# Performance work log

Hardware: AMD Instinct MI355X
Metric: run time of the kernel (lower is better)

## Reference

```python
import jax, jax.numpy as jnp
import numpy as np

B, P, CV = 2, 1024, 768
V, DNB, K = 50000, 300, 3
H = 768  # max(512, v_dim)
TOTAL_IN = CV + K * DNB + K  # include_scores=True
EPS = 1e-12


def setup_inputs() -> dict:
    key = jax.random.key(0)
    ks = jax.random.split(key, 7)
    v_seq = jax.random.normal(ks[0], (B, P, CV), dtype=jnp.float32)
    T = jax.random.normal(ks[1], (V, CV), dtype=jnp.float32)
    T_clip = T / jnp.linalg.norm(T, axis=-1, keepdims=True)  # bank rows are L2-normalized
    nb_vecs = jax.random.normal(ks[2], (V, DNB), dtype=jnp.float32)
    W1 = jax.random.normal(ks[3], (TOTAL_IN, H), dtype=jnp.float32) * (1.0 / np.sqrt(TOTAL_IN))
    b1 = jnp.zeros((H,), dtype=jnp.float32)
    W2 = jax.random.normal(ks[4], (H, CV), dtype=jnp.float32) * (1.0 / np.sqrt(H))
    b2 = jnp.zeros((CV,), dtype=jnp.float32)
    return {"v_seq": v_seq, "T_clip": T_clip, "nb_vecs": nb_vecs,
            "W1": W1, "b1": b1, "W2": W2, "b2": b2}


def _layer_norm(x, eps=1e-5):
    mu = jnp.mean(x, axis=-1, keepdims=True)
    var = jnp.var(x, axis=-1, keepdims=True)
    return (x - mu) * jax.lax.rsqrt(var + eps)


def reference(v_seq, T_clip, nb_vecs, W1, b1, W2, b2):
    # --- retrieve (no_grad in original) ---
    q = v_seq / jnp.maximum(jnp.linalg.norm(v_seq, axis=-1, keepdims=True), EPS)
    S = jnp.einsum('bpc,vc->bpv', q, T_clip)            # (B,P,V) cosine sims
    val, idx = jax.lax.top_k(S, K)                       # (B,P,K) each
    nb_sel = nb_vecs[idx]                                # gather -> (B,P,K,DNB)
    # --- fuse_concat ---
    nb_flat = nb_sel.reshape(B, P, K * DNB)
    combined = jnp.concatenate([v_seq, nb_flat, val], axis=-1)  # (B,P,TOTAL_IN)
    h = jax.nn.gelu(combined @ W1 + b1, approximate=False)      # nn.GELU default = erf
    fused = h @ W2 + b2                                          # dropout inactive (eval)
    return _layer_norm(fused)                                    # F.layer_norm, no affine
```

## Files before the change

kernel.cpp:

```cpp
#include <hip/hip_runtime.h>
#include <hip/hip_bf16.h>

typedef unsigned short u16;
typedef unsigned int u32;
typedef __attribute__((ext_vector_type(4))) unsigned short u16x4;
typedef __attribute__((ext_vector_type(8))) unsigned short u16x8;
typedef __attribute__((ext_vector_type(8))) short bf16x8;
typedef __attribute__((ext_vector_type(4))) float f32x4;

#define ROWS 2048
#define CV 768
#define VOCAB 50000
#define NPAD 50176
#define NTILES 196
#define NSEG 392
#define NSEGP 392
#define DNB 300
#define TOTAL_IN 1671
#define KPAD1 1696
#define HD 768
#define NT 12

__device__ __forceinline__ u16 f2bf(float f) {
  union { __hip_bfloat16 h; u16 u; } x;
  x.h = __float2bfloat16(f);
  return x.u;
}

__device__ __forceinline__ u16 bfkey(u16 u) {
  return (u & 0x8000) ? (u16)~u : (u16)(u | 0x8000);
}

__device__ __forceinline__ void gload16(const u16* g, const u16* l) {
  __builtin_amdgcn_global_load_lds(
      (const __attribute__((address_space(1))) void*)g,
      (__attribute__((address_space(3))) void*)l, 16, 0, 0);
}

__device__ __forceinline__ float block_sum256(float v, float* ws) {
#pragma unroll
  for (int off = 32; off > 0; off >>= 1) v += __shfl_xor(v, off, 64);
  int tid = threadIdx.x;
  if ((tid & 63) == 0) ws[tid >> 6] = v;
  __syncthreads();
  float s = ws[0] + ws[1] + ws[2] + ws[3];
  __syncthreads();
  return s;
}

__global__ __launch_bounds__(256) void normalize_kernel(
    const float* __restrict__ v_seq, float* __restrict__ q, u16* __restrict__ q16) {
  __shared__ float ws[4];
  int row = blockIdx.x, tid = threadIdx.x;
  const float* x = v_seq + (size_t)row * CV;
  float x0 = x[tid], x1 = x[tid + 256], x2 = x[tid + 512];
  float s = block_sum256(x0 * x0 + x1 * x1 + x2 * x2, ws);
  float denom = fmaxf(sqrtf(s), 1e-12f);
  float q0 = x0 / denom, q1 = x1 / denom, q2 = x2 / denom;
  float* qr = q + (size_t)row * CV;
  u16* qb = q16 + (size_t)row * CV;
  qr[tid] = q0; qr[tid + 256] = q1; qr[tid + 512] = q2;
  qb[tid] = f2bf(q0); qb[tid + 256] = f2bf(q1); qb[tid + 512] = f2bf(q2);
}

__global__ __launch_bounds__(256) void cvt_bf16_kernel(
    const float* __restrict__ src, u16* __restrict__ dst, int n4) {
  int i = blockIdx.x * 256 + threadIdx.x;
  int stride = gridDim.x * 256;
  for (; i < n4; i += stride) {
    float4 v = reinterpret_cast<const float4*>(src)[i];
    u16x4 o = {f2bf(v.x), f2bf(v.y), f2bf(v.z), f2bf(v.w)};
    reinterpret_cast<u16x4*>(dst)[i] = o;
  }
}

__global__ __launch_bounds__(256) void transpose_cvt_kernel(
    const float* __restrict__ src, u16* __restrict__ dst, int Ksrc, int ldk, int N) {
  __shared__ float tile[32][33];
  int tx = threadIdx.x & 31, ty = threadIdx.x >> 5;
  int kb = blockIdx.x * 32, nb = blockIdx.y * 32;
#pragma unroll
  for (int i = 0; i < 4; ++i) {
    int k = kb + ty + i * 8, n = nb + tx;
    tile[ty + i * 8][tx] = (k < Ksrc) ? src[(size_t)k * N + n] : 0.f;
  }
  __syncthreads();
#pragma unroll
  for (int i = 0; i < 4; ++i) {
    int n = nb + ty + i * 8, k = kb + tx;
    dst[(size_t)n * ldk + k] = f2bf(tile[tx][ty + i * 8]);
  }
}

__global__ __launch_bounds__(512, 2) void score_gemm_256(
    const u16* __restrict__ q16, const u16* __restrict__ T16,
    u16* __restrict__ S16, u16* __restrict__ segmax) {
  __shared__ __align__(16) u16 lds[65536];
  __shared__ float smx[256][4];

  int tid = threadIdx.x;
  int w = tid >> 6, lane = tid & 63;
  int wr = w >> 2, wc = w & 3;
  int l15 = lane & 15, l4 = lane >> 4;

  int bid = blockIdx.x;
  int wg = (bid & 7) * NTILES + (bid >> 3);
  int mtile = wg & 7, ntile = wg >> 3;
  int m0 = mtile * 256, n0 = ntile * 256;

  int t8 = tid >> 3;
  int jcol = (((tid & 7) ^ (t8 & 7)) << 3);
  int rowA = m0 + t8;
  int rowB0 = n0 + t8;        rowB0 = rowB0 > (VOCAB - 1) ? (VOCAB - 1) : rowB0;
  int rowB1 = n0 + 64 + t8;   rowB1 = rowB1 > (VOCAB - 1) ? (VOCAB - 1) : rowB1;
  int rowB2 = n0 + 128 + t8;  rowB2 = rowB2 > (VOCAB - 1) ? (VOCAB - 1) : rowB2;
  int rowB3 = n0 + 192 + t8;  rowB3 = rowB3 > (VOCAB - 1) ? (VOCAB - 1) : rowB3;
  int w512 = w * 512;

  int xorv = (l15 & 7) << 4;
  int l416 = l4 << 4;
  int c0 = ((l416) ^ xorv) >> 1;
  int c1 = ((64 + l416) ^ xorv) >> 1;
  int aro = (wr * 128 + l15) * 64;
  int bro = 16384 + (wc * 64 + l15) * 64;

  f32x4 acc[8][4];
#pragma unroll
  for (int i = 0; i < 8; ++i)
#pragma unroll
    for (int j = 0; j < 4; ++j) acc[i][j] = {0.f, 0.f, 0.f, 0.f};

  bf16x8 af[2][4], bfr[2][4];

#define STAGE_A(R0) gload16(q16 + (size_t)(rowA + (R0)) * CV + ktn + jcol, \
                            &lds[nbase + (R0) * 64 + w512])
#define STAGE_B0() gload16(T16 + (size_t)rowB0 * CV + ktn + jcol, &lds[nbase + 16384 + w512])
#define STAGE_B1() gload16(T16 + (size_t)rowB1 * CV + ktn + jcol, &lds[nbase + 16384 + 4096 + w512])
#define STAGE_B2() gload16(T16 + (size_t)rowB2 * CV + ktn + jcol, &lds[nbase + 16384 + 8192 + w512])
#define STAGE_B3() gload16(T16 + (size_t)rowB3 * CV + ktn + jcol, &lds[nbase + 16384 + 12288 + w512])

#define LDA4(MIB)                                                           \
  _Pragma("unroll") for (int ks = 0; ks < 2; ++ks)                          \
  _Pragma("unroll") for (int mi = 0; mi < 4; ++mi)                          \
    af[ks][mi] = *reinterpret_cast<const bf16x8*>(                          \
        &lds[cbase + aro + ((MIB) + mi) * 1024 + (ks ? c1 : c0)]);

#define LDB2(NIB)                                                           \
  _Pragma("unroll") for (int ks = 0; ks < 2; ++ks)                          \
  _Pragma("unroll") for (int ni = 0; ni < 2; ++ni)                          \
    bfr[ks][(NIB) + ni] = *reinterpret_cast<const bf16x8*>(                 \
        &lds[cbase + bro + ((NIB) + ni) * 1024 + (ks ? c1 : c0)]);

#define MFMAQ(MIB, NIB)                                                     \
  _Pragma("unroll") for (int mi = 0; mi < 4; ++mi)                          \
  _Pragma("unroll") for (int ni = 0; ni < 2; ++ni) {                        \
    acc[(MIB) + mi][(NIB) + ni] = __builtin_amdgcn_mfma_f32_16x16x32_bf16(  \
        af[0][mi], bfr[0][(NIB) + ni], acc[(MIB) + mi][(NIB) + ni], 0, 0, 0); \
    acc[(MIB) + mi][(NIB) + ni] = __builtin_amdgcn_mfma_f32_16x16x32_bf16(  \
        af[1][mi], bfr[1][(NIB) + ni], acc[(MIB) + mi][(NIB) + ni], 0, 0, 0); \
  }

  {
    int nbase = 0, ktn = 0;
    STAGE_B0(); STAGE_B1(); STAGE_B2(); STAGE_B3();
    STAGE_A(0); STAGE_A(128); STAGE_A(64); STAGE_A(192);
  }

  for (int t = 0; t < NT; ++t) {
    int cb = t & 1;
    int cbase = cb * 32768;
    int nbase = cbase ^ 32768;
    int ktn = ((t + 1 < NT) ? (t + 1) : t) * 64;

    asm volatile("s_waitcnt vmcnt(2)" ::: "memory");
    __builtin_amdgcn_s_barrier();

    LDA4(0)
    LDB2(0)
    STAGE_B0(); STAGE_B1();
    __builtin_amdgcn_s_barrier();
    __builtin_amdgcn_s_setprio(1);
    MFMAQ(0, 0)
    __builtin_amdgcn_s_setprio(0);
    __builtin_amdgcn_s_barrier();

    LDB2(2)
    STAGE_B2(); STAGE_B3();
    __builtin_amdgcn_s_barrier();
    __builtin_amdgcn_s_setprio(1);
    MFMAQ(0, 2)
    __builtin_amdgcn_s_setprio(0);
    asm volatile("s_waitcnt vmcnt(4)" ::: "memory");
    __builtin_amdgcn_s_barrier();

    LDA4(4)
    STAGE_A(0); STAGE_A(128);
    __builtin_amdgcn_s_barrier();
    __builtin_amdgcn_s_setprio(1);
    MFMAQ(4, 0)
    __builtin_amdgcn_s_setprio(0);
    __builtin_amdgcn_s_barrier();

    STAGE_A(64); STAGE_A(192);
    __builtin_amdgcn_s_setprio(1);
    MFMAQ(4, 2)
    __builtin_amdgcn_s_setprio(0);
  }
  asm volatile("s_waitcnt vmcnt(0)" ::: "memory");
  __builtin_amdgcn_s_barrier();

#pragma unroll
  for (int mi = 0; mi < 8; ++mi)
#pragma unroll
    for (int ni = 0; ni < 4; ++ni) {
      int gr = m0 + wr * 128 + mi * 16 + l4 * 4;
      int gc = n0 + wc * 64 + ni * 16 + l15;
#pragma unroll
      for (int r = 0; r < 4; ++r)
        S16[(size_t)(gr + r) * NPAD + gc] = f2bf(acc[mi][ni][r]);
    }

#pragma unroll
  for (int mi = 0; mi < 8; ++mi)
#pragma unroll
    for (int r = 0; r < 4; ++r) {
      float v = -3e38f;
#pragma unroll
      for (int ni = 0; ni < 4; ++ni) {
        bool ok = (n0 + wc * 64 + ni * 16 + l15) < VOCAB;
        v = fmaxf(v, ok ? acc[mi][ni][r] : -3e38f);
      }
#pragma unroll
      for (int d = 1; d < 16; d <<= 1) v = fmaxf(v, __shfl_xor(v, d, 64));
      if (l15 == 0) smx[wr * 128 + mi * 16 + l4 * 4 + r][wc] = v;
    }
  __syncthreads();
  if (tid < 256) {
    float s0 = fmaxf(smx[tid][0], smx[tid][1]);
    float s1 = fmaxf(smx[tid][2], smx[tid][3]);
    segmax[(size_t)(m0 + tid) * NSEGP + 2 * ntile]     = bfkey(f2bf(s0));
    segmax[(size_t)(m0 + tid) * NSEGP + 2 * ntile + 1] = bfkey(f2bf(s1));
  }
#undef STAGE_A
#undef STAGE_B0
#undef STAGE_B1
#undef STAGE_B2
#undef STAGE_B3
#undef LDA4
#undef LDB2
#undef MFMAQ
}

template <int ACT, int OUTBF>
__global__ __launch_bounds__(256) void gemm_bt(
    const u16* __restrict__ A, int lda,
    const u16* __restrict__ B, int ldb, int nclamp,
    int Kdim, const float* __restrict__ bias,
    float* __restrict__ Cf, u16* __restrict__ Cb, int ldc) {
  __shared__ __align__(16) u16 Asm[128 * 32];
  __shared__ __align__(16) u16 Bsm[128 * 32];
  int tid = threadIdx.x;
  int w = tid >> 6, lane = tid & 63;
  int wr = w >> 1, wc = w & 1;
  int m0 = blockIdx.x * 128;
  int n0 = blockIdx.y * 128;
  f32x4 acc[4][4];
#pragma unroll
  for (int i = 0; i < 4; ++i)
#pragma unroll
    for (int j = 0; j < 4; ++j) acc[i][j] = {0.f, 0.f, 0.f, 0.f};

  int r0 = tid >> 2, s0 = tid & 3;
  int b0r = n0 + r0;       b0r = b0r > nclamp ? nclamp : b0r;
  int b1r = n0 + 64 + r0;  b1r = b1r > nclamp ? nclamp : b1r;

  for (int k0 = 0; k0 < Kdim; k0 += 32) {
    __syncthreads();
    gload16(A + (size_t)(m0 + r0) * lda + k0 + s0 * 8, Asm + w * 512);
    gload16(A + (size_t)(m0 + 64 + r0) * lda + k0 + s0 * 8, Asm + 2048 + w * 512);
    gload16(B + (size_t)b0r * ldb + k0 + s0 * 8, Bsm + w * 512);
    gload16(B + (size_t)b1r * ldb + k0 + s0 * 8, Bsm + 2048 + w * 512);
    __syncthreads();
    int l15 = lane & 15, l4 = lane >> 4;
    bf16x8 af[4], bfr[4];
#pragma unroll
    for (int mi = 0; mi < 4; ++mi)
      af[mi] = *reinterpret_cast<const bf16x8*>(Asm + (wr * 64 + mi * 16 + l15) * 32 + l4 * 8);
#pragma unroll
    for (int ni = 0; ni < 4; ++ni)
      bfr[ni] = *reinterpret_cast<const bf16x8*>(Bsm + (wc * 64 + ni * 16 + l15) * 32 + l4 * 8);
#pragma unroll
    for (int mi = 0; mi < 4; ++mi)
#pragma unroll
      for (int ni = 0; ni < 4; ++ni)
        acc[mi][ni] = __builtin_amdgcn_mfma_f32_16x16x32_bf16(af[mi], bfr[ni], acc[mi][ni], 0, 0, 0);
  }

  int l15 = lane & 15, l4 = lane >> 4;
#pragma unroll
  for (int mi = 0; mi < 4; ++mi) {
#pragma unroll
    for (int ni = 0; ni < 4; ++ni) {
      int gr = m0 + wr * 64 + mi * 16 + l4 * 4;
      int gc = n0 + wc * 64 + ni * 16 + l15;
      float bv = bias ? bias[gc] : 0.f;
#pragma unroll
      for (int r = 0; r < 4; ++r) {
        float x = acc[mi][ni][r] + bv;
        if (ACT) x = 0.5f * x * (1.0f + erff(x * 0.70710678118654752f));
        size_t co = (size_t)(gr + r) * ldc + gc;
        if (OUTBF) Cb[co] = f2bf(x);
        else       Cf[co] = x;
      }
    }
  }
}

__global__ __launch_bounds__(256) void segsel_topk(
    const u16* __restrict__ segmax, const u16* __restrict__ S,
    int* __restrict__ cidx) {
  __shared__ u32 skey[448];
  __shared__ u32 winners[16];
  __shared__ u32 cl[256][16];
  int row = blockIdx.x, tid = threadIdx.x;

  if (tid < 224) {
#pragma unroll
    for (int j = 0; j < 2; ++j) {
      int s = tid * 2 + j;
      u32 k = 0;
      if (s < NSEG) k = ((u32)segmax[(size_t)row * NSEGP + s] << 9) | (u32)(511 - s);
      skey[s] = k;
    }
  }
  __syncthreads();

  if (tid < 64) {
    u32 v[7];
#pragma unroll
    for (int j = 0; j < 7; ++j) v[j] = skey[tid + 64 * j];
#pragma unroll
    for (int rd = 0; rd < 16; ++rd) {
      u32 m = v[0];
#pragma unroll
      for (int j = 1; j < 7; ++j) m = (v[j] > m) ? v[j] : m;
#pragma unroll
      for (int d = 1; d < 64; d <<= 1) {
        u32 o = (u32)__shfl_xor((int)m, d, 64);
        m = (o > m) ? o : m;
      }
#pragma unroll
      for (int j = 0; j < 7; ++j) v[j] = (v[j] == m) ? 0u : v[j];
      if (tid == 0) winners[rd] = m;
    }
  }
  __syncthreads();

  int wi = tid >> 4, off = (tid & 15) * 8;
  int seg = 511 - (int)(winners[wi] & 511);
  const u16* Sr = S + (size_t)row * NPAD + seg * 128 + off;
  u16x8 vv = *reinterpret_cast<const u16x8*>(Sr);
  u32 ck[8];
  int gbase = seg * 128 + off;
#pragma unroll
  for (int jj = 0; jj < 8; ++jj) {
    int g = gbase + jj;
    u32 c = ((u32)bfkey(vv[jj]) << 16) | (u32)(0xFFFF - g);
    ck[jj] = (g >= VOCAB) ? 0u : c;
  }
#define CE(i, j) { u32 a = ck[i], b = ck[j]; ck[i] = a > b ? a : b; ck[j] = a > b ? b : a; }
  CE(0,1) CE(2,3) CE(4,5) CE(6,7)
  CE(0,2) CE(1,3) CE(4,6) CE(5,7)
  CE(1,2) CE(5,6)
  CE(0,4) CE(1,5) CE(2,6) CE(3,7)
  CE(2,4) CE(3,5)
  CE(1,2) CE(3,4) CE(5,6)
#undef CE
#pragma unroll
  for (int k = 0; k < 8; ++k) cl[tid][k] = ck[k];
#pragma unroll
  for (int k = 8; k < 16; ++k) cl[tid][k] = 0u;
  __syncthreads();

  for (int s = 128; s >= 1; s >>= 1) {
    if (tid < s) {
      u32 ov[16];
      int pa = 0, pb = 0;
#pragma unroll
      for (int k = 0; k < 16; ++k) {
        u32 va = cl[tid][pa], vb = cl[tid + s][pb];
        bool ta = va >= vb;
        ov[k] = ta ? va : vb;
        pa += ta ? 1 : 0;
        pb += ta ? 0 : 1;
      }
#pragma unroll
      for (int k = 0; k < 16; ++k) cl[tid][k] = ov[k];
    }
    __syncthreads();
  }
  if (tid < 16) cidx[(size_t)row * 16 + tid] = 0xFFFF - (int)(cl[0][tid] & 0xFFFF);
}

__global__ __launch_bounds__(256) void rescore_kernel(
    const float* __restrict__ q, const float* __restrict__ T,
    const int* __restrict__ cidx,
    float* __restrict__ val, int* __restrict__ idx) {
  __shared__ float sex[16];
  int row = blockIdx.x, tid = threadIdx.x;
  int wv = tid >> 6, lane = tid & 63;
  const float* __restrict__ qr = q + (size_t)row * CV;
#pragma unroll
  for (int c0 = 0; c0 < 4; ++c0) {
    int c = wv + c0 * 4;
    int n = cidx[(size_t)row * 16 + c];
    const float* tr = T + (size_t)n * CV;
    float part = 0.f;
    int kb = lane * 12;
#pragma unroll
    for (int j3 = 0; j3 < 3; ++j3) {
      float4 a = *reinterpret_cast<const float4*>(tr + kb + j3 * 4);
      float4 b = *reinterpret_cast<const float4*>(qr + kb + j3 * 4);
      part += a.x * b.x + a.y * b.y + a.z * b.z + a.w * b.w;
    }
#pragma unroll
    for (int off = 32; off >= 1; off >>= 1) part += __shfl_xor(part, off, 64);
    if (lane == 0) sex[c] = part;
  }
  __syncthreads();
  if (tid == 0) {
    float xv[16]; int xi[16];
#pragma unroll
    for (int c = 0; c < 16; ++c) { xv[c] = sex[c]; xi[c] = cidx[(size_t)row * 16 + c]; }
    for (int t = 0; t < 3; ++t) {
      float bv = -__builtin_inff(); int bi = 0x7fffffff, bc = -1;
#pragma unroll
      for (int c = 0; c < 16; ++c) {
        if (xi[c] < 0) continue;
        if (xv[c] > bv || (xv[c] == bv && xi[c] < bi)) { bv = xv[c]; bi = xi[c]; bc = c; }
      }
      val[row * 3 + t] = bv;
      idx[row * 3 + t] = bi;
      xi[bc] = -1;
    }
  }
}

__global__ __launch_bounds__(256) void gather_concat_kernel(
    const float* __restrict__ v_seq, const float* __restrict__ nb,
    const float* __restrict__ val, const int* __restrict__ idx,
    u16* __restrict__ c16) {
  int row = blockIdx.x, tid = threadIdx.x;
  u16* c = c16 + (size_t)row * KPAD1;
  const float* vs = v_seq + (size_t)row * CV;
  if (tid < 192) {
    float4 v = *reinterpret_cast<const float4*>(vs + tid * 4);
    u16x4 o = {f2bf(v.x), f2bf(v.y), f2bf(v.z), f2bf(v.w)};
    *reinterpret_cast<u16x4*>(c + tid * 4) = o;
  }
  int i0 = idx[row * 3 + 0], i1 = idx[row * 3 + 1], i2 = idx[row * 3 + 2];
  if (tid < 75) {
    float4 v = *reinterpret_cast<const float4*>(nb + (size_t)i0 * DNB + tid * 4);
    u16x4 o = {f2bf(v.x), f2bf(v.y), f2bf(v.z), f2bf(v.w)};
    *reinterpret_cast<u16x4*>(c + CV + tid * 4) = o;
    v = *reinterpret_cast<const float4*>(nb + (size_t)i1 * DNB + tid * 4);
    o = {f2bf(v.x), f2bf(v.y), f2bf(v.z), f2bf(v.w)};
    *reinterpret_cast<u16x4*>(c + CV + DNB + tid * 4) = o;
    v = *reinterpret_cast<const float4*>(nb + (size_t)i2 * DNB + tid * 4);
    o = {f2bf(v.x), f2bf(v.y), f2bf(v.z), f2bf(v.w)};
    *reinterpret_cast<u16x4*>(c + CV + 2 * DNB + tid * 4) = o;
  }
  if (tid < 28) {
    int o = CV + 3 * DNB + tid;
    c[o] = (tid < 3) ? f2bf(val[row * 3 + tid]) : (u16)0;
  }
}

__global__ __launch_bounds__(256) void layernorm_kernel(float* __restrict__ C) {
  __shared__ float ws[4];
  int row = blockIdx.x, tid = threadIdx.x;
  float* x = C + (size_t)row * CV;
  float x0 = x[tid], x1 = x[tid + 256], x2 = x[tid + 512];
  float mu = block_sum256(x0 + x1 + x2, ws) * (1.0f / 768.0f);
  float d0 = x0 - mu, d1 = x1 - mu, d2 = x2 - mu;
  float var = block_sum256(d0 * d0 + d1 * d1 + d2 * d2, ws) * (1.0f / 768.0f);
  float inv = 1.0f / sqrtf(var + 1e-5f);
  x[tid] = d0 * inv; x[tid + 256] = d1 * inv; x[tid + 512] = d2 * inv;
}

extern "C" void kernel_launch(void* const* d_in, const int* in_sizes, int n_in,
                              void* d_out, int out_size, void* d_ws, size_t ws_size,
                              hipStream_t stream) {
  const float* v_seq = (const float*)d_in[0];
  const float* T = (const float*)d_in[1];
  const float* nb = (const float*)d_in[2];
  const float* W1 = (const float*)d_in[3];
  const float* b1 = (const float*)d_in[4];
  const float* W2 = (const float*)d_in[5];
  const float* b2 = (const float*)d_in[6];
  float* out = (float*)d_out;

  char* base = (char*)d_ws;
  size_t off = 0;
  auto alloc = [&](size_t bytes) -> void* {
    void* p = base + off;
    off += (bytes + 255) & ~(size_t)255;
    return p;
  };
  float* q   = (float*)alloc((size_t)ROWS * CV * 4);
  u16* q16   = (u16*)alloc((size_t)ROWS * CV * 2);
  u16* T16   = (u16*)alloc((size_t)VOCAB * CV * 2);
  u16* c16   = (u16*)alloc((size_t)ROWS * KPAD1 * 2);
  u16* h16   = (u16*)alloc((size_t)ROWS * HD * 2);
  u16* W1T   = (u16*)alloc((size_t)HD * KPAD1 * 2);
  u16* W2T   = (u16*)alloc((size_t)HD * HD * 2);
  u16* segmaxb = (u16*)alloc((size_t)ROWS * NSEGP * 2);
  int* cidx   = (int*)alloc((size_t)ROWS * 16 * 4);
  float* val  = (float*)alloc((size_t)ROWS * 3 * 4);
  int* idxb   = (int*)alloc((size_t)ROWS * 3 * 4);
  u16* S16    = (u16*)alloc((size_t)ROWS * NPAD * 2);

  normalize_kernel<<<ROWS, 256, 0, stream>>>(v_seq, q, q16);
  cvt_bf16_kernel<<<2048, 256, 0, stream>>>(T, T16, VOCAB * CV / 4);
  transpose_cvt_kernel<<<dim3(KPAD1 / 32, HD / 32), 256, 0, stream>>>(W1, W1T, TOTAL_IN, KPAD1, HD);
  transpose_cvt_kernel<<<dim3(HD / 32, HD / 32), 256, 0, stream>>>(W2, W2T, HD, HD, HD);

  score_gemm_256<<<8 * NTILES, 512, 0, stream>>>(q16, T16, S16, segmaxb);
  segsel_topk<<<ROWS, 256, 0, stream>>>(segmaxb, S16, cidx);
  rescore_kernel<<<ROWS, 256, 0, stream>>>(q, T, cidx, val, idxb);
  gather_concat_kernel<<<ROWS, 256, 0, stream>>>(v_seq, nb, val, idxb, c16);
  gemm_bt<1, 1><<<dim3(ROWS / 128, HD / 128), 256, 0, stream>>>(
      c16, KPAD1, W1T, KPAD1, HD - 1, KPAD1, b1, nullptr, h16, HD);
  gemm_bt<0, 0><<<dim3(ROWS / 128, HD / 128), 256, 0, stream>>>(
      h16, HD, W2T, HD, HD - 1, HD, b2, out, nullptr, HD);
  layernorm_kernel<<<ROWS, 256, 0, stream>>>(out);
}
```

Measured before the change: 443.8 us.

## Software-pipeline score GEMM with inline-asm LDS reads and fuse rescore with concat

Rewrites the main loop of the score GEMM so it processes two K-tiles per iteration. LDS fragments are read with inline ds_read_b128 at precomputed addresses, and explicit lgkmcnt/vmcnt waits plus sched_barriers interleave the next fragment reads and global staging with the MFMA clusters. The aim is to hide LDS and global load latency behind matrix math. Separately, the rescore and gather/concat kernels are merged so top-3 values and indices stay in shared memory, removing one launch and a global round trip. The hand-tuned wait counts and barriers are fragile: a wrong count would cause races, and forcing the schedule can raise register pressure.

```diff
diff --git a/kernel.cpp b/kernel.cpp
--- a/kernel.cpp
+++ b/kernel.cpp
@@ -117,12 +117,15 @@
   int rowB3 = n0 + 192 + t8;  rowB3 = rowB3 > (VOCAB - 1) ? (VOCAB - 1) : rowB3;
   int w512 = w * 512;
 
-  int xorv = (l15 & 7) << 4;
-  int l416 = l4 << 4;
-  int c0 = ((l416) ^ xorv) >> 1;
-  int c1 = ((64 + l416) ^ xorv) >> 1;
-  int aro = (wr * 128 + l15) * 64;
-  int bro = 16384 + (wc * 64 + l15) * 64;
+  unsigned ldsb = (unsigned)(uintptr_t)(__attribute__((address_space(3))) void*)lds;
+  int x0 = ((l4 ^ (l15 & 7)) << 4);
+  int x1 = (((4 + l4) ^ (l15 & 7)) << 4);
+  int aR = (wr * 128 + l15) * 128;
+  int bR = 32768 + (wc * 64 + l15) * 128;
+  int A0k0 = ldsb + aR + x0, A0k1 = ldsb + aR + x1;
+  int B0k0 = ldsb + bR + x0, B0k1 = ldsb + bR + x1;
+  int A1k0 = A0k0 + 65536, A1k1 = A0k1 + 65536;
+  int B1k0 = B0k0 + 65536, B1k1 = B0k1 + 65536;
 
   f32x4 acc[8][4];
 #pragma unroll
@@ -130,84 +133,97 @@
 #pragma unroll
     for (int j = 0; j < 4; ++j) acc[i][j] = {0.f, 0.f, 0.f, 0.f};
 
-  bf16x8 af[2][4], bfr[2][4];
-
-#define STAGE_A(R0) gload16(q16 + (size_t)(rowA + (R0)) * CV + ktn + jcol, \
-                            &lds[nbase + (R0) * 64 + w512])
-#define STAGE_B0() gload16(T16 + (size_t)rowB0 * CV + ktn + jcol, &lds[nbase + 16384 + w512])
-#define STAGE_B1() gload16(T16 + (size_t)rowB1 * CV + ktn + jcol, &lds[nbase + 16384 + 4096 + w512])
-#define STAGE_B2() gload16(T16 + (size_t)rowB2 * CV + ktn + jcol, &lds[nbase + 16384 + 8192 + w512])
-#define STAGE_B3() gload16(T16 + (size_t)rowB3 * CV + ktn + jcol, &lds[nbase + 16384 + 12288 + w512])
-
-#define LDA4(MIB)                                                           \
-  _Pragma("unroll") for (int ks = 0; ks < 2; ++ks)                          \
-  _Pragma("unroll") for (int mi = 0; mi < 4; ++mi)                          \
-    af[ks][mi] = *reinterpret_cast<const bf16x8*>(                          \
-        &lds[cbase + aro + ((MIB) + mi) * 1024 + (ks ? c1 : c0)]);
-
-#define LDB2(NIB)                                                           \
-  _Pragma("unroll") for (int ks = 0; ks < 2; ++ks)                          \
-  _Pragma("unroll") for (int ni = 0; ni < 2; ++ni)                          \
-    bfr[ks][(NIB) + ni] = *reinterpret_cast<const bf16x8*>(                 \
-        &lds[cbase + bro + ((NIB) + ni) * 1024 + (ks ? c1 : c0)]);
-
-#define MFMAQ(MIB, NIB)                                                     \
-  _Pragma("unroll") for (int mi = 0; mi < 4; ++mi)                          \
-  _Pragma("unroll") for (int ni = 0; ni < 2; ++ni) {                        \
-    acc[(MIB) + mi][(NIB) + ni] = __builtin_amdgcn_mfma_f32_16x16x32_bf16(  \
-        af[0][mi], bfr[0][(NIB) + ni], acc[(MIB) + mi][(NIB) + ni], 0, 0, 0); \
-    acc[(MIB) + mi][(NIB) + ni] = __builtin_amdgcn_mfma_f32_16x16x32_bf16(  \
-        af[1][mi], bfr[1][(NIB) + ni], acc[(MIB) + mi][(NIB) + ni], 0, 0, 0); \
-  }
-
-  {
-    int nbase = 0, ktn = 0;
-    STAGE_B0(); STAGE_B1(); STAGE_B2(); STAGE_B3();
-    STAGE_A(0); STAGE_A(128); STAGE_A(64); STAGE_A(192);
-  }
-
-  for (int t = 0; t < NT; ++t) {
-    int cb = t & 1;
-    int cbase = cb * 32768;
-    int nbase = cbase ^ 32768;
-    int ktn = ((t + 1 < NT) ? (t + 1) : t) * 64;
-
-    asm volatile("s_waitcnt vmcnt(2)" ::: "memory");
-    __builtin_amdgcn_s_barrier();
-
-    LDA4(0)
-    LDB2(0)
-    STAGE_B0(); STAGE_B1();
-    __builtin_amdgcn_s_barrier();
-    __builtin_amdgcn_s_setprio(1);
-    MFMAQ(0, 0)
-    __builtin_amdgcn_s_setprio(0);
-    __builtin_amdgcn_s_barrier();
-
-    LDB2(2)
-    STAGE_B2(); STAGE_B3();
-    __builtin_amdgcn_s_barrier();
-    __builtin_amdgcn_s_setprio(1);
-    MFMAQ(0, 2)
-    __builtin_amdgcn_s_setprio(0);
-    asm volatile("s_waitcnt vmcnt(4)" ::: "memory");
-    __builtin_amdgcn_s_barrier();
-
-    LDA4(4)
-    STAGE_A(0); STAGE_A(128);
-    __builtin_amdgcn_s_barrier();
-    __builtin_amdgcn_s_setprio(1);
-    MFMAQ(4, 0)
-    __builtin_amdgcn_s_setprio(0);
-    __builtin_amdgcn_s_barrier();
-
-    STAGE_A(64); STAGE_A(192);
-    __builtin_amdgcn_s_setprio(1);
-    MFMAQ(4, 2)
-    __builtin_amdgcn_s_setprio(0);
-  }
-  asm volatile("s_waitcnt vmcnt(0)" ::: "memory");
-  __builtin_amdgcn_s_barrier();
+  bf16x8 alo[2][4], ahi[2][4], b01[2][2], b23[2][2];
+
+#define STG(ptr, off16) gload16((ptr), lds + (off16))
+#define STAGE6(NB, KT)                                                        \
+  STG(q16 + (size_t)(rowA) * CV + (KT) + jcol, (NB) + w512);                  \
+  STG(q16 + (size_t)(rowA + 128) * CV + (KT) + jcol, (NB) + 8192 + w512);     \
+  STG(T16 + (size_t)rowB0 * CV + (KT) + jcol, (NB) + 16384 + w512);           \
+  STG(T16 + (size_t)rowB1 * CV + (KT) + jcol, (NB) + 16384 + 4096 + w512);    \
+  STG(T16 + (size_t)rowB2 * CV + (KT) + jcol, (NB) + 16384 + 8192 + w512);    \
+  STG(T16 + (size_t)rowB3 * CV + (KT) + jcol, (NB) + 16384 + 12288 + w512);
+#define STAGE2(NB, KT)                                                        \
+  STG(q16 + (size_t)(rowA + 64) * CV + (KT) + jcol, (NB) + 4096 + w512);      \
+  STG(q16 + (size_t)(rowA + 192) * CV + (KT) + jcol, (NB) + 12288 + w512);
+
+#define DSR(D, B, O) asm volatile("ds_read_b128 %0, %1 offset:" O : "=v"(D) : "v"(B))
+#define READ_B01(K0, K1)                                                      \
+  DSR(b01[0][0], K0, "0"); DSR(b01[0][1], K0, "2048");                        \
+  DSR(b01[1][0], K1, "0"); DSR(b01[1][1], K1, "2048");
+#define READ_B23(K0, K1)                                                      \
+  DSR(b23[0][0], K0, "4096"); DSR(b23[0][1], K0, "6144");                     \
+  DSR(b23[1][0], K1, "4096"); DSR(b23[1][1], K1, "6144");
+#define READ_ALO(K0, K1)                                                      \
+  DSR(alo[0][0], K0, "0"); DSR(alo[0][1], K0, "2048");                        \
+  DSR(alo[0][2], K0, "4096"); DSR(alo[0][3], K0, "6144");                     \
+  DSR(alo[1][0], K1, "0"); DSR(alo[1][1], K1, "2048");                        \
+  DSR(alo[1][2], K1, "4096"); DSR(alo[1][3], K1, "6144");
+#define READ_AHI(K0, K1)                                                      \
+  DSR(ahi[0][0], K0, "8192"); DSR(ahi[0][1], K0, "10240");                    \
+  DSR(ahi[0][2], K0, "12288"); DSR(ahi[0][3], K0, "14336");                   \
+  DSR(ahi[1][0], K1, "8192"); DSR(ahi[1][1], K1, "10240");                    \
+  DSR(ahi[1][2], K1, "12288"); DSR(ahi[1][3], K1, "14336");
+
+#define LGKM(N)                                                               \
+  asm volatile("s_waitcnt lgkmcnt(" N ")" ::: "memory");                      \
+  __builtin_amdgcn_sched_barrier(0)
+#define VMC(N) asm volatile("s_waitcnt vmcnt(" N ")" ::: "memory")
+#define BARX                                                                  \
+  __builtin_amdgcn_sched_barrier(0);                                          \
+  __builtin_amdgcn_s_barrier()
+
+#define CLUSTER(AA, MIB, BB, NIB)                                             \
+  __builtin_amdgcn_s_setprio(1);                                              \
+  _Pragma("unroll") for (int mi = 0; mi < 4; ++mi)                            \
+  _Pragma("unroll") for (int ni = 0; ni < 2; ++ni) {                          \
+    acc[(MIB)+mi][(NIB)+ni] = __builtin_amdgcn_mfma_f32_16x16x32_bf16(        \
+        AA[0][mi], BB[0][ni], acc[(MIB)+mi][(NIB)+ni], 0, 0, 0);              \
+    acc[(MIB)+mi][(NIB)+ni] = __builtin_amdgcn_mfma_f32_16x16x32_bf16(        \
+        AA[1][mi], BB[1][ni], acc[(MIB)+mi][(NIB)+ni], 0, 0, 0);              \
+  }                                                                           \
+  __builtin_amdgcn_s_setprio(0);
+
+  STAGE6(0, 0)
+  STAGE2(0, 0)
+  VMC("2");
+  BARX;
+  READ_ALO(A0k0, A0k1)
+  READ_B01(B0k0, B0k1)
+
+  for (int p = 0; p < 6; ++p) {
+    int kt1 = (2 * p + 1) * 64;
+    int kt2 = (p < 5) ? (2 * p + 2) * 64 : 11 * 64;
+    READ_B23(B0k0, B0k1)
+    STAGE6(32768, kt1)
+    LGKM("4"); CLUSTER(alo, 0, b01, 0) VMC("6"); BARX;
+
+    READ_AHI(A0k0, A0k1)
+    STAGE2(32768, kt1)
+    LGKM("8"); CLUSTER(alo, 0, b23, 2) BARX;
+
+    LGKM("0"); CLUSTER(ahi, 4, b23, 2) VMC("2"); BARX;
+
+    READ_ALO(A1k0, A1k1)
+    READ_B23(B1k0, B1k1)
+    CLUSTER(ahi, 4, b01, 0) BARX;
+    READ_B01(B1k0, B1k1)
+    STAGE6(0, kt2)
+    LGKM("4"); CLUSTER(alo, 0, b23, 2) VMC("6"); BARX;
+
+    READ_AHI(A1k0, A1k1)
+    STAGE2(0, kt2)
+    LGKM("8"); CLUSTER(alo, 0, b01, 0) BARX;
+
+    LGKM("0"); CLUSTER(ahi, 4, b01, 0) VMC("2"); BARX;
+
+    READ_ALO(A0k0, A0k1)
+    READ_B01(B0k0, B0k1)
+    CLUSTER(ahi, 4, b23, 2) BARX;
+  }
+  VMC("0");
+  asm volatile("s_waitcnt lgkmcnt(0)" ::: "memory");
+  __syncthreads();
 
 #pragma unroll
   for (int mi = 0; mi < 8; ++mi)
@@ -241,14 +257,18 @@
     segmax[(size_t)(m0 + tid) * NSEGP + 2 * ntile]     = bfkey(f2bf(s0));
     segmax[(size_t)(m0 + tid) * NSEGP + 2 * ntile + 1] = bfkey(f2bf(s1));
   }
-#undef STAGE_A
-#undef STAGE_B0
-#undef STAGE_B1
-#undef STAGE_B2
-#undef STAGE_B3
-#undef LDA4
-#undef LDB2
-#undef MFMAQ
+#undef STG
+#undef STAGE6
+#undef STAGE2
+#undef DSR
+#undef READ_B01
+#undef READ_B23
+#undef READ_ALO
+#undef READ_AHI
+#undef LGKM
+#undef VMC
+#undef BARX
+#undef CLUSTER
 }
 
 template <int ACT, int OUTBF>
@@ -402,11 +422,13 @@
   if (tid < 16) cidx[(size_t)row * 16 + tid] = 0xFFFF - (int)(cl[0][tid] & 0xFFFF);
 }
 
-__global__ __launch_bounds__(256) void rescore_kernel(
+__global__ __launch_bounds__(256) void rescore_concat(
     const float* __restrict__ q, const float* __restrict__ T,
-    const int* __restrict__ cidx,
-    float* __restrict__ val, int* __restrict__ idx) {
+    const int* __restrict__ cidx, const float* __restrict__ v_seq,
+    const float* __restrict__ nb, u16* __restrict__ c16) {
   __shared__ float sex[16];
+  __shared__ float sval[3];
+  __shared__ int sidx[3];
   int row = blockIdx.x, tid = threadIdx.x;
   int wv = tid >> 6, lane = tid & 63;
   const float* __restrict__ qr = q + (size_t)row * CV;
@@ -439,18 +461,12 @@
         if (xi[c] < 0) continue;
         if (xv[c] > bv || (xv[c] == bv && xi[c] < bi)) { bv = xv[c]; bi = xi[c]; bc = c; }
       }
-      val[row * 3 + t] = bv;
-      idx[row * 3 + t] = bi;
+      sval[t] = bv; sidx[t] = bi;
       xi[bc] = -1;
     }
   }
-}
-
-__global__ __launch_bounds__(256) void gather_concat_kernel(
-    const float* __restrict__ v_seq, const float* __restrict__ nb,
-    const float* __restrict__ val, const int* __restrict__ idx,
-    u16* __restrict__ c16) {
-  int row = blockIdx.x, tid = threadIdx.x;
+  __syncthreads();
+
   u16* c = c16 + (size_t)row * KPAD1;
   const float* vs = v_seq + (size_t)row * CV;
   if (tid < 192) {
@@ -458,7 +474,7 @@
     u16x4 o = {f2bf(v.x), f2bf(v.y), f2bf(v.z), f2bf(v.w)};
     *reinterpret_cast<u16x4*>(c + tid * 4) = o;
   }
-  int i0 = idx[row * 3 + 0], i1 = idx[row * 3 + 1], i2 = idx[row * 3 + 2];
+  int i0 = sidx[0], i1 = sidx[1], i2 = sidx[2];
   if (tid < 75) {
     float4 v = *reinterpret_cast<const float4*>(nb + (size_t)i0 * DNB + tid * 4);
     u16x4 o = {f2bf(v.x), f2bf(v.y), f2bf(v.z), f2bf(v.w)};
@@ -472,7 +488,7 @@
   }
   if (tid < 28) {
     int o = CV + 3 * DNB + tid;
-    c[o] = (tid < 3) ? f2bf(val[row * 3 + tid]) : (u16)0;
+    c[o] = (tid < 3) ? f2bf(sval[tid]) : (u16)0;
   }
 }
 
@@ -516,8 +532,6 @@
   u16* W2T   = (u16*)alloc((size_t)HD * HD * 2);
   u16* segmaxb = (u16*)alloc((size_t)ROWS * NSEGP * 2);
   int* cidx   = (int*)alloc((size_t)ROWS * 16 * 4);
-  float* val  = (float*)alloc((size_t)ROWS * 3 * 4);
-  int* idxb   = (int*)alloc((size_t)ROWS * 3 * 4);
   u16* S16    = (u16*)alloc((size_t)ROWS * NPAD * 2);
 
   normalize_kernel<<<ROWS, 256, 0, stream>>>(v_seq, q, q16);
@@ -527,8 +541,7 @@
 
   score_gemm_256<<<8 * NTILES, 512, 0, stream>>>(q16, T16, S16, segmaxb);
   segsel_topk<<<ROWS, 256, 0, stream>>>(segmaxb, S16, cidx);
-  rescore_kernel<<<ROWS, 256, 0, stream>>>(q, T, cidx, val, idxb);
-  gather_concat_kernel<<<ROWS, 256, 0, stream>>>(v_seq, nb, val, idxb, c16);
+  rescore_concat<<<ROWS, 256, 0, stream>>>(q, T, cidx, v_seq, nb, c16);
   gemm_bt<1, 1><<<dim3(ROWS / 128, HD / 128), 256, 0, stream>>>(
       c16, KPAD1, W1T, KPAD1, HD - 1, KPAD1, b1, nullptr, h16, HD);
   gemm_bt<0, 0><<<dim3(ROWS / 128, HD / 128), 256, 0, stream>>>(
```

After: 622.5 us. +40.3%, slower.

## Compute per-tile top-8 candidates in score GEMM epilogue instead of writing full score matrix

Applied to the files above, without the earlier changes.

The score GEMM no longer writes the full bf16 similarity matrix (about 200 MB) plus segment maxima. Each 256-column tile is staged in LDS, where every thread keeps a per-row top-8 by insertion and pairs of threads merge their lists; only 8 packed key/index candidates per row per tile go to memory. A new merge_topk kernel reduces these candidates to 16 per row. Rescoring and gather/concat are fused into one kernel that uses a stored reciprocal norm instead of a normalized fp32 copy of q. This adds serial insertion-sort work to the GEMM epilogue, but removes the large score-matrix write and reread.

```diff
diff --git a/kernel.cpp b/kernel.cpp
--- a/kernel.cpp
+++ b/kernel.cpp
@@ -13,8 +13,7 @@
 #define VOCAB 50000
 #define NPAD 50176
 #define NTILES 196
-#define NSEG 392
-#define NSEGP 392
+#define CANDW (NTILES * 8)
 #define DNB 300
 #define TOTAL_IN 1671
 #define KPAD1 1696
@@ -49,18 +48,17 @@
 }
 
 __global__ __launch_bounds__(256) void normalize_kernel(
-    const float* __restrict__ v_seq, float* __restrict__ q, u16* __restrict__ q16) {
+    const float* __restrict__ v_seq, float* __restrict__ rinv, u16* __restrict__ q16) {
   __shared__ float ws[4];
   int row = blockIdx.x, tid = threadIdx.x;
   const float* x = v_seq + (size_t)row * CV;
   float x0 = x[tid], x1 = x[tid + 256], x2 = x[tid + 512];
   float s = block_sum256(x0 * x0 + x1 * x1 + x2 * x2, ws);
   float denom = fmaxf(sqrtf(s), 1e-12f);
-  float q0 = x0 / denom, q1 = x1 / denom, q2 = x2 / denom;
-  float* qr = q + (size_t)row * CV;
+  float inv = 1.0f / denom;
   u16* qb = q16 + (size_t)row * CV;
-  qr[tid] = q0; qr[tid + 256] = q1; qr[tid + 512] = q2;
-  qb[tid] = f2bf(q0); qb[tid + 256] = f2bf(q1); qb[tid + 512] = f2bf(q2);
+  qb[tid] = f2bf(x0 * inv); qb[tid + 256] = f2bf(x1 * inv); qb[tid + 512] = f2bf(x2 * inv);
+  if (tid == 0) rinv[row] = inv;
 }
 
 __global__ __launch_bounds__(256) void cvt_bf16_kernel(
@@ -94,9 +92,8 @@
 
 __global__ __launch_bounds__(512, 2) void score_gemm_256(
     const u16* __restrict__ q16, const u16* __restrict__ T16,
-    u16* __restrict__ S16, u16* __restrict__ segmax) {
+    u32* __restrict__ cand) {
   __shared__ __align__(16) u16 lds[65536];
-  __shared__ float smx[256][4];
 
   int tid = threadIdx.x;
   int w = tid >> 6, lane = tid & 63;
@@ -207,39 +204,65 @@
     __builtin_amdgcn_s_setprio(0);
   }
   asm volatile("s_waitcnt vmcnt(0)" ::: "memory");
-  __builtin_amdgcn_s_barrier();
-
-#pragma unroll
-  for (int mi = 0; mi < 8; ++mi)
-#pragma unroll
-    for (int ni = 0; ni < 4; ++ni) {
-      int gr = m0 + wr * 128 + mi * 16 + l4 * 4;
-      int gc = n0 + wc * 64 + ni * 16 + l15;
-#pragma unroll
-      for (int r = 0; r < 4; ++r)
-        S16[(size_t)(gr + r) * NPAD + gc] = f2bf(acc[mi][ni][r]);
-    }
-
-#pragma unroll
-  for (int mi = 0; mi < 8; ++mi)
-#pragma unroll
-    for (int r = 0; r < 4; ++r) {
-      float v = -3e38f;
+  asm volatile("s_waitcnt lgkmcnt(0)" ::: "memory");
+  __syncthreads();
+
+  {
+#pragma unroll
+    for (int mi = 0; mi < 8; ++mi)
 #pragma unroll
       for (int ni = 0; ni < 4; ++ni) {
-        bool ok = (n0 + wc * 64 + ni * 16 + l15) < VOCAB;
-        v = fmaxf(v, ok ? acc[mi][ni][r] : -3e38f);
-      }
-#pragma unroll
-      for (int d = 1; d < 16; d <<= 1) v = fmaxf(v, __shfl_xor(v, d, 64));
-      if (l15 == 0) smx[wr * 128 + mi * 16 + l4 * 4 + r][wc] = v;
-    }
-  __syncthreads();
-  if (tid < 256) {
-    float s0 = fmaxf(smx[tid][0], smx[tid][1]);
-    float s1 = fmaxf(smx[tid][2], smx[tid][3]);
-    segmax[(size_t)(m0 + tid) * NSEGP + 2 * ntile]     = bfkey(f2bf(s0));
-    segmax[(size_t)(m0 + tid) * NSEGP + 2 * ntile + 1] = bfkey(f2bf(s1));
+        int lrb = wr * 128 + mi * 16 + l4 * 4;
+        int lc = wc * 64 + ni * 16 + l15;
+        int gc = n0 + lc;
+        u16* dst = lds + ((lc >> 3) * 256) * 8 + (lc & 7);
+#pragma unroll
+        for (int r = 0; r < 4; ++r) {
+          u16 k = (gc < VOCAB) ? bfkey(f2bf(acc[mi][ni][r])) : (u16)0;
+          dst[(lrb + r) * 8] = k;
+        }
+      }
+    __syncthreads();
+
+    int prow = tid >> 1, half = tid & 1;
+    u32 b[8] = {0, 0, 0, 0, 0, 0, 0, 0};
+    int gcb = ntile * 256 + half * 128;
+#pragma unroll 4
+    for (int i = 0; i < 16; ++i) {
+      u16x8 v = *reinterpret_cast<const u16x8*>(lds + ((half * 16 + i) * 256 + prow) * 8);
+#pragma unroll
+      for (int j = 0; j < 8; ++j) {
+        u32 pk = ((u32)v[j] << 16) | (0xFFFFu ^ (u32)(gcb + i * 8 + j));
+        if (pk > b[7]) {
+          b[7] = pk;
+#pragma unroll
+          for (int k = 7; k > 0; --k) {
+            if (b[k] > b[k - 1]) { u32 tt = b[k]; b[k] = b[k - 1]; b[k - 1] = tt; }
+          }
+        }
+      }
+    }
+    __syncthreads();
+    u32* ex = (u32*)lds;
+#pragma unroll
+    for (int j = 0; j < 8; ++j) ex[tid * 8 + j] = b[j];
+    __syncthreads();
+    if (!half) {
+      const u32* pb = ex + (tid + 1) * 8;
+      u32 o[8];
+      int pa = 0, pq = 0;
+#pragma unroll
+      for (int k = 0; k < 8; ++k) {
+        u32 va = b[pa], vb = pb[pq];
+        bool ta = va >= vb;
+        o[k] = ta ? va : vb;
+        pa += ta ? 1 : 0;
+        pq += ta ? 0 : 1;
+      }
+      u32* cr = cand + (size_t)(m0 + prow) * CANDW + ntile * 8;
+#pragma unroll
+      for (int k = 0; k < 8; ++k) cr[k] = o[k];
+    }
   }
 #undef STAGE_A
 #undef STAGE_B0
@@ -249,6 +272,48 @@
 #undef LDA4
 #undef LDB2
 #undef MFMAQ
+}
+
+__global__ __launch_bounds__(256) void merge_topk(
+    const u32* __restrict__ cand, int* __restrict__ cidx) {
+  __shared__ u32 cl[256][16];
+  int row = blockIdx.x, tid = threadIdx.x;
+  const u32* cr = cand + (size_t)row * CANDW;
+  u32 b[8] = {0, 0, 0, 0, 0, 0, 0, 0};
+  for (int i = tid; i < CANDW; i += 256) {
+    u32 pk = cr[i];
+    if (pk > b[7]) {
+      b[7] = pk;
+#pragma unroll
+      for (int k = 7; k > 0; --k) {
+        if (b[k] > b[k - 1]) { u32 tt = b[k]; b[k] = b[k - 1]; b[k - 1] = tt; }
+      }
+    }
+  }
+#pragma unroll
+  for (int k = 0; k < 8; ++k) cl[tid][k] = b[k];
+#pragma unroll
+  for (int k = 8; k < 16; ++k) cl[tid][k] = 0u;
+  __syncthreads();
+
+  for (int s = 128; s >= 1; s >>= 1) {
+    if (tid < s) {
+      u32 ov[16];
+      int pa = 0, pb = 0;
+#pragma unroll
+      for (int k = 0; k < 16; ++k) {
+        u32 va = cl[tid][pa], vb = cl[tid + s][pb];
+        bool ta = va >= vb;
+        ov[k] = ta ? va : vb;
+        pa += ta ? 1 : 0;
+        pb += ta ? 0 : 1;
+      }
+#pragma unroll
+      for (int k = 0; k < 16; ++k) cl[tid][k] = ov[k];
+    }
+    __syncthreads();
+  }
+  if (tid < 16) cidx[(size_t)row * 16 + tid] = (int)(0xFFFFu ^ (cl[0][tid] & 0xFFFFu));
 }
 
 template <int ACT, int OUTBF>
@@ -316,100 +381,17 @@
   }
 }
 
-__global__ __launch_bounds__(256) void segsel_topk(
-    const u16* __restrict__ segmax, const u16* __restrict__ S,
-    int* __restrict__ cidx) {
-  __shared__ u32 skey[448];
-  __shared__ u32 winners[16];
-  __shared__ u32 cl[256][16];
-  int row = blockIdx.x, tid = threadIdx.x;
-
-  if (tid < 224) {
-#pragma unroll
-    for (int j = 0; j < 2; ++j) {
-      int s = tid * 2 + j;
-      u32 k = 0;
-      if (s < NSEG) k = ((u32)segmax[(size_t)row * NSEGP + s] << 9) | (u32)(511 - s);
-      skey[s] = k;
-    }
-  }
-  __syncthreads();
-
-  if (tid < 64) {
-    u32 v[7];
-#pragma unroll
-    for (int j = 0; j < 7; ++j) v[j] = skey[tid + 64 * j];
-#pragma unroll
-    for (int rd = 0; rd < 16; ++rd) {
-      u32 m = v[0];
-#pragma unroll
-      for (int j = 1; j < 7; ++j) m = (v[j] > m) ? v[j] : m;
-#pragma unroll
-      for (int d = 1; d < 64; d <<= 1) {
-        u32 o = (u32)__shfl_xor((int)m, d, 64);
-        m = (o > m) ? o : m;
-      }
-#pragma unroll
-      for (int j = 0; j < 7; ++j) v[j] = (v[j] == m) ? 0u : v[j];
-      if (tid == 0) winners[rd] = m;
-    }
-  }
-  __syncthreads();
-
-  int wi = tid >> 4, off = (tid & 15) * 8;
-  int seg = 511 - (int)(winners[wi] & 511);
-  const u16* Sr = S + (size_t)row * NPAD + seg * 128 + off;
-  u16x8 vv = *reinterpret_cast<const u16x8*>(Sr);
-  u32 ck[8];
-  int gbase = seg * 128 + off;
-#pragma unroll
-  for (int jj = 0; jj < 8; ++jj) {
-    int g = gbase + jj;
-    u32 c = ((u32)bfkey(vv[jj]) << 16) | (u32)(0xFFFF - g);
-    ck[jj] = (g >= VOCAB) ? 0u : c;
-  }
-#define CE(i, j) { u32 a = ck[i], b = ck[j]; ck[i] = a > b ? a : b; ck[j] = a > b ? b : a; }
-  CE(0,1) CE(2,3) CE(4,5) CE(6,7)
-  CE(0,2) CE(1,3) CE(4,6) CE(5,7)
-  CE(1,2) CE(5,6)
-  CE(0,4) CE(1,5) CE(2,6) CE(3,7)
-  CE(2,4) CE(3,5)
-  CE(1,2) CE(3,4) CE(5,6)
-#undef CE
-#pragma unroll
-  for (int k = 0; k < 8; ++k) cl[tid][k] = ck[k];
-#pragma unroll
-  for (int k = 8; k < 16; ++k) cl[tid][k] = 0u;
-  __syncthreads();
-
-  for (int s = 128; s >= 1; s >>= 1) {
-    if (tid < s) {
-      u32 ov[16];
-      int pa = 0, pb = 0;
-#pragma unroll
-      for (int k = 0; k < 16; ++k) {
-        u32 va = cl[tid][pa], vb = cl[tid + s][pb];
-        bool ta = va >= vb;
-        ov[k] = ta ? va : vb;
-        pa += ta ? 1 : 0;
-        pb += ta ? 0 : 1;
-      }
-#pragma unroll
-      for (int k = 0; k < 16; ++k) cl[tid][k] = ov[k];
-    }
-    __syncthreads();
-  }
-  if (tid < 16) cidx[(size_t)row * 16 + tid] = 0xFFFF - (int)(cl[0][tid] & 0xFFFF);
-}
-
-__global__ __launch_bounds__(256) void rescore_kernel(
-    const float* __restrict__ q, const float* __restrict__ T,
-    const int* __restrict__ cidx,
-    float* __restrict__ val, int* __restrict__ idx) {
+__global__ __launch_bounds__(256) void rescore_concat(
+    const float* __restrict__ v_seq, const float* __restrict__ rinv,
+    const float* __restrict__ T, const int* __restrict__ cidx,
+    const float* __restrict__ nb, u16* __restrict__ c16) {
   __shared__ float sex[16];
+  __shared__ float sval[3];
+  __shared__ int sidx[3];
   int row = blockIdx.x, tid = threadIdx.x;
   int wv = tid >> 6, lane = tid & 63;
-  const float* __restrict__ qr = q + (size_t)row * CV;
+  const float* __restrict__ qr = v_seq + (size_t)row * CV;
+  float ri = rinv[row];
 #pragma unroll
   for (int c0 = 0; c0 < 4; ++c0) {
     int c = wv + c0 * 4;
@@ -425,7 +407,7 @@
     }
 #pragma unroll
     for (int off = 32; off >= 1; off >>= 1) part += __shfl_xor(part, off, 64);
-    if (lane == 0) sex[c] = part;
+    if (lane == 0) sex[c] = part * ri;
   }
   __syncthreads();
   if (tid == 0) {
@@ -439,26 +421,19 @@
         if (xi[c] < 0) continue;
         if (xv[c] > bv || (xv[c] == bv && xi[c] < bi)) { bv = xv[c]; bi = xi[c]; bc = c; }
       }
-      val[row * 3 + t] = bv;
-      idx[row * 3 + t] = bi;
+      sval[t] = bv; sidx[t] = bi;
       xi[bc] = -1;
     }
   }
-}
-
-__global__ __launch_bounds__(256) void gather_concat_kernel(
-    const float* __restrict__ v_seq, const float* __restrict__ nb,
-    const float* __restrict__ val, const int* __restrict__ idx,
-    u16* __restrict__ c16) {
-  int row = blockIdx.x, tid = threadIdx.x;
+  __syncthreads();
+
   u16* c = c16 + (size_t)row * KPAD1;
-  const float* vs = v_seq + (size_t)row * CV;
   if (tid < 192) {
-    float4 v = *reinterpret_cast<const float4*>(vs + tid * 4);
+    float4 v = *reinterpret_cast<const float4*>(qr + tid * 4);
     u16x4 o = {f2bf(v.x), f2bf(v.y), f2bf(v.z), f2bf(v.w)};
     *reinterpret_cast<u16x4*>(c + tid * 4) = o;
   }
-  int i0 = idx[row * 3 + 0], i1 = idx[row * 3 + 1], i2 = idx[row * 3 + 2];
+  int i0 = sidx[0], i1 = sidx[1], i2 = sidx[2];
   if (tid < 75) {
     float4 v = *reinterpret_cast<const float4*>(nb + (size_t)i0 * DNB + tid * 4);
     u16x4 o = {f2bf(v.x), f2bf(v.y), f2bf(v.z), f2bf(v.w)};
@@ -472,7 +447,7 @@
   }
   if (tid < 28) {
     int o = CV + 3 * DNB + tid;
-    c[o] = (tid < 3) ? f2bf(val[row * 3 + tid]) : (u16)0;
+    c[o] = (tid < 3) ? f2bf(sval[tid]) : (u16)0;
   }
 }
 
@@ -507,28 +482,24 @@
     off += (bytes + 255) & ~(size_t)255;
     return p;
   };
-  float* q   = (float*)alloc((size_t)ROWS * CV * 4);
+  float* rinv = (float*)alloc((size_t)ROWS * 4);
   u16* q16   = (u16*)alloc((size_t)ROWS * CV * 2);
   u16* T16   = (u16*)alloc((size_t)VOCAB * CV * 2);
   u16* c16   = (u16*)alloc((size_t)ROWS * KPAD1 * 2);
   u16* h16   = (u16*)alloc((size_t)ROWS * HD * 2);
   u16* W1T   = (u16*)alloc((size_t)HD * KPAD1 * 2);
   u16* W2T   = (u16*)alloc((size_t)HD * HD * 2);
-  u16* segmaxb = (u16*)alloc((size_t)ROWS * NSEGP * 2);
-  int* cidx   = (int*)alloc((size_t)ROWS * 16 * 4);
-  float* val  = (float*)alloc((size_t)ROWS * 3 * 4);
-  int* idxb   = (int*)alloc((size_t)ROWS * 3 * 4);
-  u16* S16    = (u16*)alloc((size_t)ROWS * NPAD * 2);
-
-  normalize_kernel<<<ROWS, 256, 0, stream>>>(v_seq, q, q16);
+  u32* cand  = (u32*)alloc((size_t)ROWS * CANDW * 4);
+  int* cidx  = (int*)alloc((size_t)ROWS * 16 * 4);
+
+  normalize_kernel<<<ROWS, 256, 0, stream>>>(v_seq, rinv, q16);
   cvt_bf16_kernel<<<2048, 256, 0, stream>>>(T, T16, VOCAB * CV / 4);
   transpose_cvt_kernel<<<dim3(KPAD1 / 32, HD / 32), 256, 0, stream>>>(W1, W1T, TOTAL_IN, KPAD1, HD);
   transpose_cvt_kernel<<<dim3(HD / 32, HD / 32), 256, 0, stream>>>(W2, W2T, HD, HD, HD);
 
-  score_gemm_256<<<8 * NTILES, 512, 0, stream>>>(q16, T16, S16, segmaxb);
-  segsel_topk<<<ROWS, 256, 0, stream>>>(segmaxb, S16, cidx);
-  rescore_kernel<<<ROWS, 256, 0, stream>>>(q, T, cidx, val, idxb);
-  gather_concat_kernel<<<ROWS, 256, 0, stream>>>(v_seq, nb, val, idxb, c16);
+  score_gemm_256<<<8 * NTILES, 512, 0, stream>>>(q16, T16, cand);
+  merge_topk<<<ROWS, 256, 0, stream>>>(cand, cidx);
+  rescore_concat<<<ROWS, 256, 0, stream>>>(v_seq, rinv, T, cidx, nb, c16);
   gemm_bt<1, 1><<<dim3(ROWS / 128, HD / 128), 256, 0, stream>>>(
       c16, KPAD1, W1T, KPAD1, HD - 1, KPAD1, b1, nullptr, h16, HD);
   gemm_bt<0, 0><<<dim3(ROWS / 128, HD / 128), 256, 0, stream>>>(
```

New measurement: 694.9 us. 1.57x slower.
